# Performance work log

Hardware: AMD Instinct MI355X
Metric: run time of the kernel (lower is better)

Reference implementation:

```python
import jax, jax.numpy as jnp
import numpy as np

B, S, D = 1, 2048, 1024          # batch, seq, n_embd
E, F = 16, 1024                  # n_routed_experts, moe_intermediate_size
NG, TKG, K = 4, 2, 4             # n_group, topk_group, num_experts_per_tok
NSH = 2                          # n_shared_experts
SCALE = 2.5                      # routed_scaling_factor
STD = 0.02
EPG = E // NG                    # experts per group


def setup_inputs() -> dict:
    key = jax.random.key(0)
    ks = jax.random.split(key, 8)
    return {
        "hidden_states": jax.random.normal(ks[0], (B, S, D), jnp.float32),
        "router_w": jax.random.normal(ks[1], (E, D), jnp.float32) * STD,   # gate.weight
        "bias": jnp.zeros((E,), jnp.float32),                              # e_score_correction_bias
        "gate_w": jax.random.normal(ks[2], (E, D, F), jnp.float32) * STD,  # per-expert gate_proj (transposed)
        "up_w": jax.random.normal(ks[3], (E, D, F), jnp.float32) * STD,    # per-expert up_proj
        "down_w": jax.random.normal(ks[4], (E, F, D), jnp.float32) * STD,  # per-expert down_proj
        "sh_gate_w": jax.random.normal(ks[5], (D, NSH * F), jnp.float32) * STD,
        "sh_up_w": jax.random.normal(ks[6], (D, NSH * F), jnp.float32) * STD,
        "sh_down_w": jax.random.normal(ks[7], (NSH * F, D), jnp.float32) * STD,
    }


def _route(x_flat, router_w, bias):
    # x_flat: [T, D] -> topk_idx [T, K], topk_w [T, K]
    logits = x_flat.astype(jnp.float32) @ router_w.T          # [T, E]
    scores = jax.nn.sigmoid(logits)
    s = scores + bias[None, :]                                # scores_for_choice
    sg = s.reshape(-1, NG, EPG)
    group_score = jax.lax.top_k(sg, 2)[0].sum(-1)             # sum of top-2 per group [T, NG]
    gidx = jax.lax.top_k(group_score, TKG)[1]                 # [T, TKG]
    gmask = jnp.sum(jax.nn.one_hot(gidx, NG, dtype=jnp.float32), axis=1) > 0   # [T, NG]
    emask = jnp.repeat(gmask, EPG, axis=1)                    # [T, E]
    masked = jnp.where(emask, s, -1.0)
    topk_idx = jax.lax.top_k(masked, K)[1]                    # [T, K]
    tw = jnp.take_along_axis(scores, topk_idx, axis=1)        # gather raw sigmoid scores
    tw = tw / (tw.sum(-1, keepdims=True) + 1e-20)             # norm_topk_prob
    tw = tw * SCALE
    return topk_idx, tw


def reference(hidden_states, router_w, bias, gate_w, up_w, down_w,
              sh_gate_w, sh_up_w, sh_down_w):
    x = hidden_states.reshape(-1, D)                          # [T, D]
    topk_idx, tw = _route(x, router_w, bias)
    # combine weights per (token, expert): scatter-add of topk weights
    combine = (jax.nn.one_hot(topk_idx, E, dtype=tw.dtype) * tw[..., None]).sum(1)  # [T, E]
    # per-expert SwiGLU MLPs (dense dispatch, masked combine == index_add semantics)
    h = jnp.einsum('td,edf->etf', x, gate_w)                  # [E, T, F]
    u = jnp.einsum('td,edf->etf', x, up_w)
    y = jnp.einsum('etf,efd->etd', jax.nn.silu(h) * u, down_w)  # [E, T, D]
    routed = jnp.einsum('etd,te->td', y, combine)             # weighted combine
    # shared experts
    sh = (jax.nn.silu(x @ sh_gate_w) * (x @ sh_up_w)) @ sh_down_w
    return (routed + sh).reshape(hidden_states.shape)
```

## Files before the change

### kernel.cpp

```cpp
#include <hip/hip_runtime.h>
#include <cstdint>
#include <cstddef>


#define T_TOK 2048
#define DIM   1024
#define NEXP  16
#define FDIM  1024
#define MAXTILES 80
#define MAXSLOTS (MAXTILES*128)

typedef __bf16 bf16x8_t __attribute__((ext_vector_type(8)));
typedef float  f32x4_t  __attribute__((ext_vector_type(4)));
typedef unsigned short ushort8_t __attribute__((ext_vector_type(8)));
typedef unsigned short ushort4_t __attribute__((ext_vector_type(4)));

#define OFF_XB     (0UL)
#define OFF_GATET  (4UL<<20)
#define OFF_UPT    (36UL<<20)
#define OFF_DOWNT  (68UL<<20)
#define OFF_SHGT   (100UL<<20)
#define OFF_SHUT   (104UL<<20)
#define OFF_SHDT   (108UL<<20)
#define OFF_H      (112UL<<20)
#define OFF_U      (132UL<<20)
#define OFF_YSLOT  (152UL<<20)
#define OFF_CTRL   (172UL<<20)
#define CT_OFFSETS  128
#define CT_NTILES   192
#define CT_TILEEXP  256
#define CT_SLOTTOK  4096
#define CT_TKSLOT   49152
#define CT_TOPKIDX  81920
#define CT_TOPKW    114688

__device__ __forceinline__ unsigned short f2bf(float f) {
  __bf16 h = (__bf16)f;
  return __builtin_bit_cast(unsigned short, h);
}
__device__ __forceinline__ float bf2f(unsigned short u) {
  unsigned int v = ((unsigned int)u) << 16;
  return __builtin_bit_cast(float, v);
}
__device__ __forceinline__ void gld16(const void* g, void* l) {
  __builtin_amdgcn_global_load_lds(
      (const __attribute__((address_space(1))) void*)(g),
      (__attribute__((address_space(3))) void*)(l), 16, 0, 0);
}

__global__ void k_cvt(const float* __restrict__ src, unsigned short* __restrict__ dst, int n4) {
  int i = blockIdx.x * blockDim.x + threadIdx.x;
  if (i >= n4) return;
  float4 v = ((const float4*)src)[i];
  ushort4_t o;
  o[0] = f2bf(v.x); o[1] = f2bf(v.y); o[2] = f2bf(v.z); o[3] = f2bf(v.w);
  ((ushort4_t*)dst)[i] = o;
}

__global__ void k_transpose(const float* __restrict__ src, unsigned short* __restrict__ dst,
                            int R, int C) {
  __shared__ unsigned short tile[64 * 68];
  long b = blockIdx.z;
  src += b * (long)R * C;
  dst += b * (long)R * C;
  int cT = blockIdx.x * 64, rT = blockIdx.y * 64;
  int t = threadIdx.x;
  int rb = t >> 4, cb = t & 15;
  float f[4][4];
#pragma unroll
  for (int i = 0; i < 4; i++) {
    float4 v = *(const float4*)(src + (long)(rT + 4 * rb + i) * C + cT + 4 * cb);
    f[i][0] = v.x; f[i][1] = v.y; f[i][2] = v.z; f[i][3] = v.w;
  }
#pragma unroll
  for (int j = 0; j < 4; j++) {
    ushort4_t o;
    o[0] = f2bf(f[0][j]); o[1] = f2bf(f[1][j]); o[2] = f2bf(f[2][j]); o[3] = f2bf(f[3][j]);
    int c = 4 * cb + j;
    *(ushort4_t*)&tile[c * 68 + 4 * rb] = o;
  }
  __syncthreads();
#pragma unroll
  for (int p = 0; p < 2; p++) {
    int q = t + 256 * p;
    int c = q >> 3, r0 = (q & 7) * 8;
    ushort4_t lo = *(const ushort4_t*)&tile[c * 68 + r0];
    ushort4_t hi = *(const ushort4_t*)&tile[c * 68 + r0 + 4];
    ushort8_t w8 = {lo[0], lo[1], lo[2], lo[3], hi[0], hi[1], hi[2], hi[3]};
    *(ushort8_t*)(dst + (long)(cT + c) * R + rT + r0) = w8;
  }
}

__global__ __launch_bounds__(256) void k_router(
    const float* __restrict__ x, const float* __restrict__ rw,
    const float* __restrict__ bias, int* __restrict__ topk_idx,
    float* __restrict__ topk_w) {
  int t = blockIdx.x, tid = threadIdx.x;
  int wv = tid >> 6, lane = tid & 63;
  float4 xv = ((const float4*)(x + (size_t)t * DIM))[tid];
  float part[NEXP];
#pragma unroll
  for (int e = 0; e < NEXP; e++) {
    float4 wr = ((const float4*)(rw + (size_t)e * DIM))[tid];
    part[e] = xv.x * wr.x + xv.y * wr.y + xv.z * wr.z + xv.w * wr.w;
  }
  __shared__ float wsum_s[4 * NEXP];
#pragma unroll
  for (int e = 0; e < NEXP; e++) {
    float v = part[e];
#pragma unroll
    for (int off = 32; off; off >>= 1) v += __shfl_xor(v, off, 64);
    if (lane == 0) wsum_s[wv * NEXP + e] = v;
  }
  __syncthreads();
  if (tid == 0) {
    float r_sc[NEXP], r_s[NEXP];
#pragma unroll
    for (int e = 0; e < NEXP; e++) {
      float logit = wsum_s[e] + wsum_s[NEXP + e] + wsum_s[2 * NEXP + e] +
                    wsum_s[3 * NEXP + e];
      float sc = 1.f / (1.f + expf(-logit));
      r_sc[e] = sc;
      r_s[e] = sc + bias[e];
    }
    float gs[4];
#pragma unroll
    for (int g = 0; g < 4; g++) {
      float m1 = -1e30f, m2 = -1e30f;
#pragma unroll
      for (int j = 0; j < 4; j++) {
        float v = r_s[g * 4 + j];
        if (v > m1) { m2 = m1; m1 = v; } else if (v > m2) m2 = v;
      }
      gs[g] = m1 + m2;
    }
    int g1 = 0;
    for (int g = 1; g < 4; g++) if (gs[g] > gs[g1]) g1 = g;
    int g2 = -1;
    for (int g = 0; g < 4; g++) { if (g == g1) continue; if (g2 < 0 || gs[g] > gs[g2]) g2 = g; }
    int taken = 0, idx[4];
    float w[4], wsum = 1e-20f;
#pragma unroll
    for (int k = 0; k < 4; k++) {
      float best = -1e30f; int bi = 0;
#pragma unroll
      for (int e2 = 0; e2 < 16; e2++) {
        if (taken & (1 << e2)) continue;
        int g = e2 >> 2;
        float v = (g == g1 || g == g2) ? r_s[e2] : -1.f;
        if (v > best) { best = v; bi = e2; }
      }
      taken |= 1 << bi; idx[k] = bi;
    }
#pragma unroll
    for (int k = 0; k < 4; k++) { w[k] = r_sc[idx[k]]; wsum += w[k]; }
    float sc2 = 2.5f / wsum;
#pragma unroll
    for (int k = 0; k < 4; k++) {
      topk_idx[t * 4 + k] = idx[k];
      topk_w[t * 4 + k] = w[k] * sc2;
    }
  }
}

__global__ __launch_bounds__(256) void k_route_post(
    const int* __restrict__ topk_idx, int* __restrict__ offsets,
    int* __restrict__ tile_expert, int* __restrict__ n_tiles,
    int* __restrict__ slot_token, int* __restrict__ tk_slot) {
  __shared__ int cnt[NEXP][257];
  __shared__ int offs[NEXP], tot[NEXP];
  int tid = threadIdx.x;
  int4 ent[8];
#pragma unroll
  for (int i = 0; i < 8; i++) ent[i] = ((const int4*)topk_idx)[tid * 8 + i];
  int lc[NEXP];
#pragma unroll
  for (int j = 0; j < NEXP; j++) lc[j] = 0;
#pragma unroll
  for (int i = 0; i < 8; i++) {
    int es[4] = {ent[i].x, ent[i].y, ent[i].z, ent[i].w};
#pragma unroll
    for (int k = 0; k < 4; k++)
#pragma unroll
      for (int j = 0; j < NEXP; j++) lc[j] += (es[k] == j) ? 1 : 0;
  }
#pragma unroll
  for (int j = 0; j < NEXP; j++) cnt[j][tid] = lc[j];
  __syncthreads();
  if (tid < NEXP) {
    int base = 0;
    for (int c = 0; c < 256; c += 8) {
      int v[8];
#pragma unroll
      for (int i = 0; i < 8; i++) v[i] = cnt[tid][c + i];
#pragma unroll
      for (int i = 0; i < 8; i++) { cnt[tid][c + i] = base; base += v[i]; }
    }
    tot[tid] = base;
  }
  __syncthreads();
  if (tid == 0) {
    int cum = 0, tt = 0;
    for (int e = 0; e < NEXP; e++) {
      offs[e] = cum;
      offsets[e] = cum;
      int nt = (tot[e] + 127) >> 7;
      for (int i = 0; i < nt; i++) tile_expert[tt++] = e;
      cum += nt << 7;
    }
    n_tiles[0] = tt;
  }
  __syncthreads();
  for (int e = 0; e < NEXP; e++) {
    int s0 = offs[e] + tot[e];
    int s1 = offs[e] + (((tot[e] + 127) >> 7) << 7);
    for (int s = s0 + tid; s < s1; s += 256) slot_token[s] = -1;
  }
  int lcur[NEXP];
#pragma unroll
  for (int j = 0; j < NEXP; j++) lcur[j] = offs[j] + cnt[j][tid];
#pragma unroll
  for (int i = 0; i < 8; i++) {
    int t = tid * 8 + i;
    int es[4] = {ent[i].x, ent[i].y, ent[i].z, ent[i].w};
#pragma unroll
    for (int k = 0; k < 4; k++) {
      int e = es[k], pos = 0;
#pragma unroll
      for (int j = 0; j < NEXP; j++) pos += (e == j) ? lcur[j] : 0;
#pragma unroll
      for (int j = 0; j < NEXP; j++) lcur[j] += (e == j) ? 1 : 0;
      slot_token[pos] = t;
      tk_slot[t * 4 + k] = pos;
    }
  }
}

template <int MODE>
__global__ __launch_bounds__(256, 2) void k_gemm(
    const unsigned short* __restrict__ Abase, const unsigned short* __restrict__ B0,
    const unsigned short* __restrict__ B1, unsigned short* __restrict__ O0,
    float* __restrict__ OF,
    const int* __restrict__ slot_token, const int* __restrict__ tile_expert,
    const int* __restrict__ n_tiles) {
  constexpr bool FUSED = (MODE == 0 || MODE == 2);
  constexpr int KT = (MODE == 3) ? 32 : 32;
  constexpr int AW = (MODE == 3) ? 2048 : 1024;
  constexpr int BW = (MODE == 3) ? 2048 : 1024;
  constexpr int OW = (MODE == 2) ? 2048 : 1024;

  int nx = blockIdx.x, bt = blockIdx.y;
  if (MODE == 0 || MODE == 1) { if (bt >= n_tiles[0]) return; }
  int n0 = nx * 128;
  const unsigned short *Bg, *Bu = nullptr;
  if (MODE == 0) { int e = tile_expert[bt]; Bg = B0 + (size_t)e * 1024 * 1024; Bu = B1 + (size_t)e * 1024 * 1024; }
  else if (MODE == 1) { int e = tile_expert[bt]; Bg = B0 + (size_t)e * 1024 * 1024; }
  else if (MODE == 2) { Bg = B0; Bu = B1; }
  else { Bg = B0; }

  __shared__ unsigned short sA[128 * 32];
  __shared__ unsigned short sBg[128 * 32];
  __shared__ unsigned short sBu[FUSED ? 128 * 32 : 1];

  int tid = threadIdx.x;
  int w = tid >> 6, L = tid & 63;
  int c0 = w * 128 + L, c1 = c0 + 64;
  int ar0 = c0 >> 2, ar1 = c1 >> 2;
  int ch0 = (c0 & 3) ^ (ar0 & 3), ch1 = (c1 & 3) ^ (ar1 & 3);
  long arow0, arow1;
  if (MODE == 0) {
    int t0 = slot_token[bt * 128 + ar0]; if (t0 < 0) t0 = 0;
    int t1 = slot_token[bt * 128 + ar1]; if (t1 < 0) t1 = 0;
    arow0 = t0; arow1 = t1;
  } else {
    arow0 = bt * 128 + ar0; arow1 = bt * 128 + ar1;
  }
  long kbase = (MODE == 3) ? (long)blockIdx.z * 1024 : 0;
  const char* aA = (const char*)(Abase + arow0 * AW + kbase) + ch0 * 16;
  const char* aB = (const char*)(Abase + arow1 * AW + kbase) + ch1 * 16;
  const char* gA = (const char*)(Bg + (size_t)(n0 + ar0) * BW + kbase) + ch0 * 16;
  const char* gB = (const char*)(Bg + (size_t)(n0 + ar1) * BW + kbase) + ch1 * 16;
  const char* uA = FUSED ? (const char*)(Bu + (size_t)(n0 + ar0) * BW) + ch0 * 16 : nullptr;
  const char* uB = FUSED ? (const char*)(Bu + (size_t)(n0 + ar1) * BW) + ch1 * 16 : nullptr;
  char* dA0 = (char*)sA + (w * 128) * 16;
  char* dA1 = (char*)sA + (w * 128 + 64) * 16;
  char* dG0 = (char*)sBg + (w * 128) * 16;
  char* dG1 = (char*)sBg + (w * 128 + 64) * 16;
  char* dU0 = (char*)sBu + (w * 128) * 16;
  char* dU1 = (char*)sBu + (w * 128 + 64) * 16;

  f32x4_t accg[4][4], accu[4][4];
#pragma unroll
  for (int i = 0; i < 4; i++)
#pragma unroll
    for (int j = 0; j < 4; j++) {
      accg[i][j] = f32x4_t{0.f, 0.f, 0.f, 0.f};
      if (FUSED) accu[i][j] = f32x4_t{0.f, 0.f, 0.f, 0.f};
    }

  int mb = (w >> 1) * 64, nb = (w & 1) * 64;
  int lr = L & 15, quad = L >> 4;
  int sw = ((quad ^ (lr & 3)) << 3);

  for (int kt = 0; kt < KT; ++kt) {
    gld16(aA, dA0); gld16(aB, dA1);
    gld16(gA, dG0); gld16(gB, dG1);
    if (FUSED) { gld16(uA, dU0); gld16(uB, dU1); }
    aA += 64; aB += 64; gA += 64; gB += 64;
    if (FUSED) { uA += 64; uB += 64; }
    __syncthreads();
    bf16x8_t af[4], bg[4], bu[4];
#pragma unroll
    for (int i = 0; i < 4; i++) af[i] = *(const bf16x8_t*)(sA + (mb + 16 * i + lr) * 32 + sw);
#pragma unroll
    for (int i = 0; i < 4; i++) bg[i] = *(const bf16x8_t*)(sBg + (nb + 16 * i + lr) * 32 + sw);
    if (FUSED) {
#pragma unroll
      for (int i = 0; i < 4; i++) bu[i] = *(const bf16x8_t*)(sBu + (nb + 16 * i + lr) * 32 + sw);
    }
#pragma unroll
    for (int i = 0; i < 4; i++)
#pragma unroll
      for (int j = 0; j < 4; j++) {
        accg[i][j] = __builtin_amdgcn_mfma_f32_16x16x32_bf16(af[i], bg[j], accg[i][j], 0, 0, 0);
        if (FUSED)
          accu[i][j] = __builtin_amdgcn_mfma_f32_16x16x32_bf16(af[i], bu[j], accu[i][j], 0, 0, 0);
      }
    __syncthreads();
  }

#pragma unroll
  for (int i = 0; i < 4; i++) {
    int rowb = bt * 128 + mb + 16 * i + quad * 4;
#pragma unroll
    for (int j = 0; j < 4; j++) {
      int col = n0 + nb + 16 * j + lr;
#pragma unroll
      for (int r = 0; r < 4; r++) {
        float h = accg[i][j][r];
        if (FUSED) {
          float u = accu[i][j][r];
          float act = h / (1.f + __expf(-h)) * u;
          O0[(size_t)(rowb + r) * OW + col] = f2bf(act);
        } else if (MODE == 1) {
          O0[(size_t)(rowb + r) * OW + col] = f2bf(h);
        } else {
          OF[(size_t)blockIdx.z * (T_TOK * 1024) + (size_t)(rowb + r) * 1024 + col] = h;
        }
      }
    }
  }
}

__global__ void k_gather(float* __restrict__ out, const float* __restrict__ partial,
                         const unsigned short* __restrict__ yslot,
                         const int* __restrict__ tk_slot, const float* __restrict__ topk_w) {
  int t = blockIdx.x, tid = threadIdx.x;
  int4 sl = ((const int4*)tk_slot)[t];
  float4 wv = ((const float4*)topk_w)[t];
  int d = 4 * tid;
  float4 p0 = *(const float4*)(partial + (size_t)t * 1024 + d);
  float4 p1 = *(const float4*)(partial + (size_t)(T_TOK * 1024) + (size_t)t * 1024 + d);
  float4 o = {p0.x + p1.x, p0.y + p1.y, p0.z + p1.z, p0.w + p1.w};
  const int s[4] = {sl.x, sl.y, sl.z, sl.w};
  const float wk[4] = {wv.x, wv.y, wv.z, wv.w};
#pragma unroll
  for (int k = 0; k < 4; k++) {
    ushort4_t y = *(const ushort4_t*)(yslot + (size_t)s[k] * 1024 + d);
    o.x += wk[k] * bf2f(y[0]);
    o.y += wk[k] * bf2f(y[1]);
    o.z += wk[k] * bf2f(y[2]);
    o.w += wk[k] * bf2f(y[3]);
  }
  *(float4*)(out + (size_t)t * 1024 + d) = o;
}

extern "C" void kernel_launch(void* const* d_in, const int* in_sizes, int n_in,
                              void* d_out, int out_size, void* d_ws, size_t ws_size,
                              hipStream_t stream) {
  const float* x = (const float*)d_in[0];
  const float* rw = (const float*)d_in[1];
  const float* bias = (const float*)d_in[2];
  const float* gw = (const float*)d_in[3];
  const float* uw = (const float*)d_in[4];
  const float* dw = (const float*)d_in[5];
  const float* sg = (const float*)d_in[6];
  const float* su = (const float*)d_in[7];
  const float* sd = (const float*)d_in[8];
  float* out = (float*)d_out;
  char* ws = (char*)d_ws;

  unsigned short* xb    = (unsigned short*)(ws + OFF_XB);
  unsigned short* gateT = (unsigned short*)(ws + OFF_GATET);
  unsigned short* upT   = (unsigned short*)(ws + OFF_UPT);
  unsigned short* downT = (unsigned short*)(ws + OFF_DOWNT);
  unsigned short* shGT  = (unsigned short*)(ws + OFF_SHGT);
  unsigned short* shUT  = (unsigned short*)(ws + OFF_SHUT);
  unsigned short* shDT  = (unsigned short*)(ws + OFF_SHDT);
  unsigned short* Hbuf  = (unsigned short*)(ws + OFF_H);
  float*          part  = (float*)(ws + OFF_U);
  unsigned short* yslot = (unsigned short*)(ws + OFF_YSLOT);
  char* ctrl = ws + OFF_CTRL;
  int* offsets_    = (int*)(ctrl + CT_OFFSETS);
  int* n_tiles     = (int*)(ctrl + CT_NTILES);
  int* tile_expert = (int*)(ctrl + CT_TILEEXP);
  int* slot_token  = (int*)(ctrl + CT_SLOTTOK);
  int* tk_slot     = (int*)(ctrl + CT_TKSLOT);
  int* topk_idx    = (int*)(ctrl + CT_TOPKIDX);
  float* topk_w    = (float*)(ctrl + CT_TOPKW);

  k_cvt<<<2048, 256, 0, stream>>>(x, xb, T_TOK * DIM / 4);
  k_transpose<<<dim3(16, 16, 16), 256, 0, stream>>>(gw, gateT, 1024, 1024);
  k_transpose<<<dim3(16, 16, 16), 256, 0, stream>>>(uw, upT, 1024, 1024);
  k_transpose<<<dim3(16, 16, 16), 256, 0, stream>>>(dw, downT, 1024, 1024);
  k_transpose<<<dim3(32, 16, 1), 256, 0, stream>>>(sg, shGT, 1024, 2048);
  k_transpose<<<dim3(32, 16, 1), 256, 0, stream>>>(su, shUT, 1024, 2048);
  k_transpose<<<dim3(16, 32, 1), 256, 0, stream>>>(sd, shDT, 2048, 1024);
  k_router<<<2048, 256, 0, stream>>>(x, rw, bias, topk_idx, topk_w);
  k_route_post<<<1, 256, 0, stream>>>(topk_idx, offsets_, tile_expert, n_tiles,
                                      slot_token, tk_slot);
  k_gemm<0><<<dim3(8, MAXTILES), 256, 0, stream>>>(xb, gateT, upT, Hbuf, nullptr,
                                                   slot_token, tile_expert, n_tiles);
  k_gemm<1><<<dim3(8, MAXTILES), 256, 0, stream>>>(Hbuf, downT, nullptr, yslot, nullptr,
                                                   slot_token, tile_expert, n_tiles);
  k_gemm<2><<<dim3(16, 16), 256, 0, stream>>>(xb, shGT, shUT, Hbuf, nullptr,
                                              slot_token, tile_expert, n_tiles);
  k_gemm<3><<<dim3(8, 16, 2), 256, 0, stream>>>(Hbuf, shDT, nullptr, nullptr, part,
                                                slot_token, tile_expert, n_tiles);
  k_gather<<<2048, 256, 0, stream>>>(out, part, yslot, tk_slot, topk_w);
}
```

Before: 475.3 us.

## Merge shared-expert GEMMs into routed expert gate/up and down launches

Replaces four GEMM launches with two kernels. Each kernel handles routed tiles and shared-expert tiles in one grid, with the shared experts treated as two extra 1024-wide experts. The goal is to fill the GPU better and cut the launch and tail overhead of the small shared-expert GEMMs. In exchange, the workspace layout changes: the partial buffer now overlaps xb and the shared weights at offset 0, and the shared down-projection writes two partial slices.

```diff
diff --git a/kernel.cpp b/kernel.cpp
--- a/kernel.cpp
+++ b/kernel.cpp
@@ -6,9 +6,10 @@
 #define T_TOK 2048
 #define DIM   1024
 #define NEXP  16
-#define FDIM  1024
 #define MAXTILES 80
-#define MAXSLOTS (MAXTILES*128)
+#define SH_TILES 32
+#define GRID_Y (MAXTILES + SH_TILES)
+#define ABASE_SH 10240
 
 typedef __bf16 bf16x8_t __attribute__((ext_vector_type(8)));
 typedef float  f32x4_t  __attribute__((ext_vector_type(4)));
@@ -16,16 +17,16 @@
 typedef unsigned short ushort4_t __attribute__((ext_vector_type(4)));
 
 #define OFF_XB     (0UL)
-#define OFF_GATET  (4UL<<20)
-#define OFF_UPT    (36UL<<20)
-#define OFF_DOWNT  (68UL<<20)
-#define OFF_SHGT   (100UL<<20)
-#define OFF_SHUT   (104UL<<20)
+#define OFF_SHGT   (4UL<<20)
+#define OFF_SHUT   (8UL<<20)
+#define OFF_GATET  (12UL<<20)
+#define OFF_UPT    (44UL<<20)
+#define OFF_DOWNT  (76UL<<20)
 #define OFF_SHDT   (108UL<<20)
-#define OFF_H      (112UL<<20)
-#define OFF_U      (132UL<<20)
-#define OFF_YSLOT  (152UL<<20)
-#define OFF_CTRL   (172UL<<20)
+#define OFF_ACT    (112UL<<20)
+#define OFF_YSLOT  (140UL<<20)
+#define OFF_PART   (0UL)
+#define OFF_CTRL   (160UL<<20)
 #define CT_OFFSETS  128
 #define CT_NTILES   192
 #define CT_TILEEXP  256
@@ -236,31 +237,36 @@
   }
 }
 
-template <int MODE>
-__global__ __launch_bounds__(256, 2) void k_gemm(
-    const unsigned short* __restrict__ Abase, const unsigned short* __restrict__ B0,
-    const unsigned short* __restrict__ B1, unsigned short* __restrict__ O0,
-    float* __restrict__ OF,
+__global__ __launch_bounds__(256, 2) void k_gateup(
+    const unsigned short* __restrict__ xb, const unsigned short* __restrict__ gateT,
+    const unsigned short* __restrict__ upT, const unsigned short* __restrict__ shGT,
+    const unsigned short* __restrict__ shUT, unsigned short* __restrict__ act,
     const int* __restrict__ slot_token, const int* __restrict__ tile_expert,
     const int* __restrict__ n_tiles) {
-  constexpr bool FUSED = (MODE == 0 || MODE == 2);
-  constexpr int KT = (MODE == 3) ? 32 : 32;
-  constexpr int AW = (MODE == 3) ? 2048 : 1024;
-  constexpr int BW = (MODE == 3) ? 2048 : 1024;
-  constexpr int OW = (MODE == 2) ? 2048 : 1024;
-
   int nx = blockIdx.x, bt = blockIdx.y;
-  if (MODE == 0 || MODE == 1) { if (bt >= n_tiles[0]) return; }
+  int NT = n_tiles[0];
+  bool routed = bt < NT;
+  const unsigned short *Bg, *Bu;
+  int actbase, tokbase = 0;
+  if (routed) {
+    int e = tile_expert[bt];
+    Bg = gateT + ((size_t)e << 20);
+    Bu = upT + ((size_t)e << 20);
+    actbase = bt * 128;
+  } else {
+    int st = bt - NT;
+    if (st >= SH_TILES) return;
+    int se = st >> 4, tt = st & 15;
+    Bg = shGT + ((size_t)se << 20);
+    Bu = shUT + ((size_t)se << 20);
+    actbase = ABASE_SH + se * T_TOK + tt * 128;
+    tokbase = tt * 128;
+  }
   int n0 = nx * 128;
-  const unsigned short *Bg, *Bu = nullptr;
-  if (MODE == 0) { int e = tile_expert[bt]; Bg = B0 + (size_t)e * 1024 * 1024; Bu = B1 + (size_t)e * 1024 * 1024; }
-  else if (MODE == 1) { int e = tile_expert[bt]; Bg = B0 + (size_t)e * 1024 * 1024; }
-  else if (MODE == 2) { Bg = B0; Bu = B1; }
-  else { Bg = B0; }
 
   __shared__ unsigned short sA[128 * 32];
   __shared__ unsigned short sBg[128 * 32];
-  __shared__ unsigned short sBu[FUSED ? 128 * 32 : 1];
+  __shared__ unsigned short sBu[128 * 32];
 
   int tid = threadIdx.x;
   int w = tid >> 6, L = tid & 63;
@@ -268,20 +274,19 @@
   int ar0 = c0 >> 2, ar1 = c1 >> 2;
   int ch0 = (c0 & 3) ^ (ar0 & 3), ch1 = (c1 & 3) ^ (ar1 & 3);
   long arow0, arow1;
-  if (MODE == 0) {
+  if (routed) {
     int t0 = slot_token[bt * 128 + ar0]; if (t0 < 0) t0 = 0;
     int t1 = slot_token[bt * 128 + ar1]; if (t1 < 0) t1 = 0;
     arow0 = t0; arow1 = t1;
   } else {
-    arow0 = bt * 128 + ar0; arow1 = bt * 128 + ar1;
-  }
-  long kbase = (MODE == 3) ? (long)blockIdx.z * 1024 : 0;
-  const char* aA = (const char*)(Abase + arow0 * AW + kbase) + ch0 * 16;
-  const char* aB = (const char*)(Abase + arow1 * AW + kbase) + ch1 * 16;
-  const char* gA = (const char*)(Bg + (size_t)(n0 + ar0) * BW + kbase) + ch0 * 16;
-  const char* gB = (const char*)(Bg + (size_t)(n0 + ar1) * BW + kbase) + ch1 * 16;
-  const char* uA = FUSED ? (const char*)(Bu + (size_t)(n0 + ar0) * BW) + ch0 * 16 : nullptr;
-  const char* uB = FUSED ? (const char*)(Bu + (size_t)(n0 + ar1) * BW) + ch1 * 16 : nullptr;
+    arow0 = tokbase + ar0; arow1 = tokbase + ar1;
+  }
+  const char* aA = (const char*)(xb + arow0 * 1024) + ch0 * 16;
+  const char* aB = (const char*)(xb + arow1 * 1024) + ch1 * 16;
+  const char* gA = (const char*)(Bg + (size_t)(n0 + ar0) * 1024) + ch0 * 16;
+  const char* gB = (const char*)(Bg + (size_t)(n0 + ar1) * 1024) + ch1 * 16;
+  const char* uA = (const char*)(Bu + (size_t)(n0 + ar0) * 1024) + ch0 * 16;
+  const char* uB = (const char*)(Bu + (size_t)(n0 + ar1) * 1024) + ch1 * 16;
   char* dA0 = (char*)sA + (w * 128) * 16;
   char* dA1 = (char*)sA + (w * 128 + 64) * 16;
   char* dG0 = (char*)sBg + (w * 128) * 16;
@@ -295,58 +300,138 @@
 #pragma unroll
     for (int j = 0; j < 4; j++) {
       accg[i][j] = f32x4_t{0.f, 0.f, 0.f, 0.f};
-      if (FUSED) accu[i][j] = f32x4_t{0.f, 0.f, 0.f, 0.f};
+      accu[i][j] = f32x4_t{0.f, 0.f, 0.f, 0.f};
     }
 
   int mb = (w >> 1) * 64, nb = (w & 1) * 64;
   int lr = L & 15, quad = L >> 4;
   int sw = ((quad ^ (lr & 3)) << 3);
 
-  for (int kt = 0; kt < KT; ++kt) {
+  for (int kt = 0; kt < 32; ++kt) {
     gld16(aA, dA0); gld16(aB, dA1);
     gld16(gA, dG0); gld16(gB, dG1);
-    if (FUSED) { gld16(uA, dU0); gld16(uB, dU1); }
-    aA += 64; aB += 64; gA += 64; gB += 64;
-    if (FUSED) { uA += 64; uB += 64; }
+    gld16(uA, dU0); gld16(uB, dU1);
+    aA += 64; aB += 64; gA += 64; gB += 64; uA += 64; uB += 64;
     __syncthreads();
     bf16x8_t af[4], bg[4], bu[4];
 #pragma unroll
     for (int i = 0; i < 4; i++) af[i] = *(const bf16x8_t*)(sA + (mb + 16 * i + lr) * 32 + sw);
 #pragma unroll
     for (int i = 0; i < 4; i++) bg[i] = *(const bf16x8_t*)(sBg + (nb + 16 * i + lr) * 32 + sw);
-    if (FUSED) {
-#pragma unroll
-      for (int i = 0; i < 4; i++) bu[i] = *(const bf16x8_t*)(sBu + (nb + 16 * i + lr) * 32 + sw);
-    }
+#pragma unroll
+    for (int i = 0; i < 4; i++) bu[i] = *(const bf16x8_t*)(sBu + (nb + 16 * i + lr) * 32 + sw);
 #pragma unroll
     for (int i = 0; i < 4; i++)
 #pragma unroll
       for (int j = 0; j < 4; j++) {
         accg[i][j] = __builtin_amdgcn_mfma_f32_16x16x32_bf16(af[i], bg[j], accg[i][j], 0, 0, 0);
-        if (FUSED)
-          accu[i][j] = __builtin_amdgcn_mfma_f32_16x16x32_bf16(af[i], bu[j], accu[i][j], 0, 0, 0);
+        accu[i][j] = __builtin_amdgcn_mfma_f32_16x16x32_bf16(af[i], bu[j], accu[i][j], 0, 0, 0);
       }
     __syncthreads();
   }
 
 #pragma unroll
   for (int i = 0; i < 4; i++) {
-    int rowb = bt * 128 + mb + 16 * i + quad * 4;
+    int rowb = actbase + mb + 16 * i + quad * 4;
 #pragma unroll
     for (int j = 0; j < 4; j++) {
       int col = n0 + nb + 16 * j + lr;
 #pragma unroll
       for (int r = 0; r < 4; r++) {
         float h = accg[i][j][r];
-        if (FUSED) {
-          float u = accu[i][j][r];
-          float act = h / (1.f + __expf(-h)) * u;
-          O0[(size_t)(rowb + r) * OW + col] = f2bf(act);
-        } else if (MODE == 1) {
-          O0[(size_t)(rowb + r) * OW + col] = f2bf(h);
-        } else {
-          OF[(size_t)blockIdx.z * (T_TOK * 1024) + (size_t)(rowb + r) * 1024 + col] = h;
-        }
+        float u = accu[i][j][r];
+        float a = h / (1.f + __expf(-h)) * u;
+        act[(size_t)(rowb + r) * 1024 + col] = f2bf(a);
+      }
+    }
+  }
+}
+
+__global__ __launch_bounds__(256, 2) void k_down(
+    const unsigned short* __restrict__ act, const unsigned short* __restrict__ downT,
+    const unsigned short* __restrict__ shDT, unsigned short* __restrict__ yslot,
+    float* __restrict__ part, const int* __restrict__ tile_expert,
+    const int* __restrict__ n_tiles) {
+  int nx = blockIdx.x, bt = blockIdx.y;
+  int NT = n_tiles[0];
+  bool routed = bt < NT;
+  const unsigned short* B;
+  size_t bstride;
+  int abase, obase, se = 0;
+  if (routed) {
+    int e = tile_expert[bt];
+    B = downT + ((size_t)e << 20);
+    bstride = 1024;
+    abase = bt * 128;
+    obase = bt * 128;
+  } else {
+    int st = bt - NT;
+    if (st >= SH_TILES) return;
+    se = st >> 4;
+    int tt = st & 15;
+    B = shDT + se * 1024;
+    bstride = 2048;
+    abase = ABASE_SH + se * T_TOK + tt * 128;
+    obase = tt * 128;
+  }
+  int n0 = nx * 128;
+
+  __shared__ unsigned short sA[128 * 32];
+  __shared__ unsigned short sB[128 * 32];
+
+  int tid = threadIdx.x;
+  int w = tid >> 6, L = tid & 63;
+  int c0 = w * 128 + L, c1 = c0 + 64;
+  int ar0 = c0 >> 2, ar1 = c1 >> 2;
+  int ch0 = (c0 & 3) ^ (ar0 & 3), ch1 = (c1 & 3) ^ (ar1 & 3);
+  const char* aA = (const char*)(act + (size_t)(abase + ar0) * 1024) + ch0 * 16;
+  const char* aB = (const char*)(act + (size_t)(abase + ar1) * 1024) + ch1 * 16;
+  const char* bA = (const char*)(B + (size_t)(n0 + ar0) * bstride) + ch0 * 16;
+  const char* bB = (const char*)(B + (size_t)(n0 + ar1) * bstride) + ch1 * 16;
+  char* dA0 = (char*)sA + (w * 128) * 16;
+  char* dA1 = (char*)sA + (w * 128 + 64) * 16;
+  char* dB0 = (char*)sB + (w * 128) * 16;
+  char* dB1 = (char*)sB + (w * 128 + 64) * 16;
+
+  f32x4_t acc[4][4];
+#pragma unroll
+  for (int i = 0; i < 4; i++)
+#pragma unroll
+    for (int j = 0; j < 4; j++) acc[i][j] = f32x4_t{0.f, 0.f, 0.f, 0.f};
+
+  int mb = (w >> 1) * 64, nb = (w & 1) * 64;
+  int lr = L & 15, quad = L >> 4;
+  int sw = ((quad ^ (lr & 3)) << 3);
+
+  for (int kt = 0; kt < 32; ++kt) {
+    gld16(aA, dA0); gld16(aB, dA1);
+    gld16(bA, dB0); gld16(bB, dB1);
+    aA += 64; aB += 64; bA += 64; bB += 64;
+    __syncthreads();
+    bf16x8_t af[4], bf[4];
+#pragma unroll
+    for (int i = 0; i < 4; i++) af[i] = *(const bf16x8_t*)(sA + (mb + 16 * i + lr) * 32 + sw);
+#pragma unroll
+    for (int i = 0; i < 4; i++) bf[i] = *(const bf16x8_t*)(sB + (nb + 16 * i + lr) * 32 + sw);
+#pragma unroll
+    for (int i = 0; i < 4; i++)
+#pragma unroll
+      for (int j = 0; j < 4; j++)
+        acc[i][j] = __builtin_amdgcn_mfma_f32_16x16x32_bf16(af[i], bf[j], acc[i][j], 0, 0, 0);
+    __syncthreads();
+  }
+
+#pragma unroll
+  for (int i = 0; i < 4; i++) {
+    int rowb = obase + mb + 16 * i + quad * 4;
+#pragma unroll
+    for (int j = 0; j < 4; j++) {
+      int col = n0 + nb + 16 * j + lr;
+#pragma unroll
+      for (int r = 0; r < 4; r++) {
+        float v = acc[i][j][r];
+        if (routed) yslot[(size_t)(rowb + r) * 1024 + col] = f2bf(v);
+        else part[(size_t)se * (T_TOK * 1024) + (size_t)(rowb + r) * 1024 + col] = v;
       }
     }
   }
@@ -391,15 +476,15 @@
   char* ws = (char*)d_ws;
 
   unsigned short* xb    = (unsigned short*)(ws + OFF_XB);
+  unsigned short* shGT  = (unsigned short*)(ws + OFF_SHGT);
+  unsigned short* shUT  = (unsigned short*)(ws + OFF_SHUT);
   unsigned short* gateT = (unsigned short*)(ws + OFF_GATET);
   unsigned short* upT   = (unsigned short*)(ws + OFF_UPT);
   unsigned short* downT = (unsigned short*)(ws + OFF_DOWNT);
-  unsigned short* shGT  = (unsigned short*)(ws + OFF_SHGT);
-  unsigned short* shUT  = (unsigned short*)(ws + OFF_SHUT);
   unsigned short* shDT  = (unsigned short*)(ws + OFF_SHDT);
-  unsigned short* Hbuf  = (unsigned short*)(ws + OFF_H);
-  float*          part  = (float*)(ws + OFF_U);
+  unsigned short* act   = (unsigned short*)(ws + OFF_ACT);
   unsigned short* yslot = (unsigned short*)(ws + OFF_YSLOT);
+  float*          part  = (float*)(ws + OFF_PART);
   char* ctrl = ws + OFF_CTRL;
   int* offsets_    = (int*)(ctrl + CT_OFFSETS);
   int* n_tiles     = (int*)(ctrl + CT_NTILES);
@@ -419,13 +504,9 @@
   k_router<<<2048, 256, 0, stream>>>(x, rw, bias, topk_idx, topk_w);
   k_route_post<<<1, 256, 0, stream>>>(topk_idx, offsets_, tile_expert, n_tiles,
                                       slot_token, tk_slot);
-  k_gemm<0><<<dim3(8, MAXTILES), 256, 0, stream>>>(xb, gateT, upT, Hbuf, nullptr,
-                                                   slot_token, tile_expert, n_tiles);
-  k_gemm<1><<<dim3(8, MAXTILES), 256, 0, stream>>>(Hbuf, downT, nullptr, yslot, nullptr,
-                                                   slot_token, tile_expert, n_tiles);
-  k_gemm<2><<<dim3(16, 16), 256, 0, stream>>>(xb, shGT, shUT, Hbuf, nullptr,
-                                              slot_token, tile_expert, n_tiles);
-  k_gemm<3><<<dim3(8, 16, 2), 256, 0, stream>>>(Hbuf, shDT, nullptr, nullptr, part,
+  k_gateup<<<dim3(8, GRID_Y), 256, 0, stream>>>(xb, gateT, upT, shGT, shUT, act,
                                                 slot_token, tile_expert, n_tiles);
+  k_down<<<dim3(8, GRID_Y), 256, 0, stream>>>(act, downT, shDT, yslot, part,
+                                              tile_expert, n_tiles);
   k_gather<<<2048, 256, 0, stream>>>(out, part, yslot, tk_slot, topk_w);
 }
```

Result: faster. 433.1 us (-8.9%).
